# Kernel optimization log

Hardware: AMD Instinct MI355X
Metric: run time of the kernel (lower is better)

## Reference

```python
import jax, jax.numpy as jnp
import numpy as np

BATCH = 4194304
ACT_DIM = 8


def setup_inputs() -> dict:
    key = jax.random.key(0)
    x = jax.random.normal(key, (BATCH, ACT_DIM), dtype=jnp.float32)
    # clamp_params = [[lower, upper]] exactly as in the torch module
    clamp_params = jnp.array([[-0.15, 0.15]], dtype=jnp.float32)
    return {"x": x, "clamp_params": clamp_params}


def reference(x, clamp_params):
    # CVXPY layer solves: argmin_y ||y - x||^2  s.t.  lo <= y <= hi
    # whose exact solution is the box projection (clamp).
    lo = clamp_params[:, 0:1]  # [1,1] broadcasts over [B, A]
    hi = clamp_params[:, 1:2]
    return jnp.clip(x, lo, hi)
```

## Files before the change

### kernel.cpp

```cpp
#include <hip/hip_runtime.h>


typedef float f32x4 __attribute__((ext_vector_type(4)));

__device__ __forceinline__ f32x4 clamp4(f32x4 v, float lo, float hi) {
    v.x = fminf(fmaxf(v.x, lo), hi);
    v.y = fminf(fmaxf(v.y, lo), hi);
    v.z = fminf(fmaxf(v.z, lo), hi);
    v.w = fminf(fmaxf(v.w, lo), hi);
    return v;
}

__global__ void __launch_bounds__(256) clamp_kernel(
    const f32x4* __restrict__ x,
    const float* __restrict__ cp,
    f32x4* __restrict__ out,
    int n4)
{
    const float lo = cp[0];
    const float hi = cp[1];
    const int stride = gridDim.x * blockDim.x;
    int i = blockIdx.x * blockDim.x + threadIdx.x;

    for (; i + 3 * stride < n4; i += 4 * stride) {
        f32x4 v0 = x[i];
        f32x4 v1 = x[i + stride];
        f32x4 v2 = x[i + 2 * stride];
        f32x4 v3 = x[i + 3 * stride];
        out[i]              = clamp4(v0, lo, hi);
        out[i + stride]     = clamp4(v1, lo, hi);
        out[i + 2 * stride] = clamp4(v2, lo, hi);
        out[i + 3 * stride] = clamp4(v3, lo, hi);
    }
    for (; i < n4; i += stride) {
        out[i] = clamp4(x[i], lo, hi);
    }
}

extern "C" void kernel_launch(void* const* d_in, const int* in_sizes, int n_in,
                              void* d_out, int out_size, void* d_ws, size_t ws_size,
                              hipStream_t stream)
{
    const f32x4* x = (const f32x4*)d_in[0];
    const float* cp = (const float*)d_in[1];
    f32x4* out = (f32x4*)d_out;

    const int n = in_sizes[0];
    const int n4 = n / 4;

    const int block = 256;
    int grid = 2048;
    const int needed = (n4 + block - 1) / block;
    if (grid > needed) grid = needed;
    if (grid < 1) grid = 1;

    clamp_kernel<<<grid, block, 0, stream>>>(x, cp, out, n4);
}
```

Baseline: 237.9 us.

## Replace grid-stride loop with one-shot blocks processing eight vectors per thread

Drops the fixed 2048-block grid-stride loop and launches enough blocks to cover the input once. Each thread issues eight independent 16-byte loads before storing the clamped results. The goal is more bytes in flight and less loop overhead on a bandwidth-bound elementwise op. In exchange it uses more registers per thread and launches many more blocks, with a guarded tail path.

After: 228.2 us. 4.1% less time.

```diff
diff --git a/kernel.cpp b/kernel.cpp
--- a/kernel.cpp
+++ b/kernel.cpp
@@ -2,6 +2,9 @@
 
 
 typedef float f32x4 __attribute__((ext_vector_type(4)));
+
+#define PT 8
+#define BLOCK 256
 
 __device__ __forceinline__ f32x4 clamp4(f32x4 v, float lo, float hi) {
     v.x = fminf(fmaxf(v.x, lo), hi);
@@ -11,7 +14,7 @@
     return v;
 }
 
-__global__ void __launch_bounds__(256) clamp_kernel(
+__global__ void __launch_bounds__(BLOCK) clamp_kernel(
     const f32x4* __restrict__ x,
     const float* __restrict__ cp,
     f32x4* __restrict__ out,
@@ -19,21 +22,23 @@
 {
     const float lo = cp[0];
     const float hi = cp[1];
-    const int stride = gridDim.x * blockDim.x;
-    int i = blockIdx.x * blockDim.x + threadIdx.x;
+    const int base = blockIdx.x * (BLOCK * PT) + threadIdx.x;
 
-    for (; i + 3 * stride < n4; i += 4 * stride) {
-        f32x4 v0 = x[i];
-        f32x4 v1 = x[i + stride];
-        f32x4 v2 = x[i + 2 * stride];
-        f32x4 v3 = x[i + 3 * stride];
-        out[i]              = clamp4(v0, lo, hi);
-        out[i + stride]     = clamp4(v1, lo, hi);
-        out[i + 2 * stride] = clamp4(v2, lo, hi);
-        out[i + 3 * stride] = clamp4(v3, lo, hi);
-    }
-    for (; i < n4; i += stride) {
-        out[i] = clamp4(x[i], lo, hi);
+    if (base + (PT - 1) * BLOCK < n4) {
+        f32x4 v[PT];
+#pragma unroll
+        for (int k = 0; k < PT; ++k)
+            v[k] = x[base + k * BLOCK];
+#pragma unroll
+        for (int k = 0; k < PT; ++k)
+            out[base + k * BLOCK] = clamp4(v[k], lo, hi);
+    } else {
+#pragma unroll
+        for (int k = 0; k < PT; ++k) {
+            int idx = base + k * BLOCK;
+            if (idx < n4)
+                out[idx] = clamp4(x[idx], lo, hi);
+        }
     }
 }
 
@@ -48,11 +53,8 @@
     const int n = in_sizes[0];
     const int n4 = n / 4;
 
-    const int block = 256;
-    int grid = 2048;
-    const int needed = (n4 + block - 1) / block;
-    if (grid > needed) grid = needed;
-    if (grid < 1) grid = 1;
+    const int per_block = BLOCK * PT;
+    const int grid = (n4 + per_block - 1) / per_block;
 
-    clamp_kernel<<<grid, block, 0, stream>>>(x, cp, out, n4);
+    clamp_kernel<<<grid, BLOCK, 0, stream>>>(x, cp, out, n4);
 }
```
